# Kernel optimization log

Measured on AMD Instinct MI355X. Metric: run time of the kernel, lower is better.

Reference implementation:

```python
import jax, jax.numpy as jnp
import numpy as np

N, E, H, D = 50000, 200000, 4, 64  # nodes, directed input edges, heads, hidden_dim
NODE_IN, EDGE_IN = 6, 4


def _ln(x, g, b):
    m = x.mean(-1, keepdims=True)
    v = ((x - m) ** 2).mean(-1, keepdims=True)
    return (x - m) / jnp.sqrt(v + 1e-5) * g + b


def setup_inputs() -> dict:
    key = jax.random.key(0)
    ks = iter(jax.random.split(key, 48))
    def w(i, o):
        return jax.random.normal(next(ks), (i, o), jnp.float32) / np.sqrt(i)
    def b(o):
        return jnp.zeros((o,), jnp.float32)
    return {
        "x": jax.random.normal(next(ks), (N, NODE_IN), jnp.float32),
        "edge_attr": jax.random.normal(next(ks), (E, EDGE_IN), jnp.float32),
        "ne_w1": w(NODE_IN, D), "ne_b1": b(D), "ne_w2": w(D, D), "ne_b2": b(D),
        "ee_w1": w(EDGE_IN, D), "ee_b1": b(D), "ee_w2": w(D, D), "ee_b2": b(D),
        "lnc_g": jnp.ones((2 * D,), jnp.float32), "lnc_b": jnp.zeros((2 * D,), jnp.float32),
        "tq_w": w(2 * D, H * D), "tq_b": b(H * D),
        "tk_w": w(2 * D, H * D), "tk_b": b(H * D),
        "tv_w": w(2 * D, H * D), "tv_b": b(H * D),
        "ts_w": w(2 * D, H * D), "ts_b": b(H * D),
        "lnt_g": jnp.ones((H * D,), jnp.float32), "lnt_b": jnp.zeros((H * D,), jnp.float32),
        "pn_w": w(H * D, D), "pn_b": b(D),
        "pe_w": w(H * D, D), "pe_b": b(D),
        "ec_w1": w(2 * D, D), "ec_b1": b(D), "ec_w2": w(D, 1), "ec_b2": b(1),
        "edge_index": jax.random.randint(next(ks), (2, E), 0, N),
    }


def _forward(x, edge_index, edge_attr, ne_w1, ne_b1, ne_w2, ne_b2,
             ee_w1, ee_b1, ee_w2, ee_b2, lnc_g, lnc_b,
             tq_w, tq_b, tk_w, tk_b, tv_w, tv_b, ts_w, ts_b,
             lnt_g, lnt_b, pn_w, pn_b, pe_w, pe_b,
             ec_w1, ec_b1, ec_w2, ec_b2):
    # bidirectionalize edges
    send = jnp.concatenate([edge_index[0], edge_index[1]])   # [2E]
    recv = jnp.concatenate([edge_index[1], edge_index[0]])   # [2E]
    ea_bi = jnp.concatenate([edge_attr, edge_attr], axis=0)  # [2E, EDGE_IN]
    # 2-layer ReLU MLP encoders (make_mlp with default ReLU output activation)
    node = jax.nn.relu(jax.nn.relu(x @ ne_w1 + ne_b1) @ ne_w2 + ne_b2)        # [N, D]
    edge = jax.nn.relu(jax.nn.relu(ea_bi @ ee_w1 + ee_b1) @ ee_w2 + ee_b2)    # [2E, D]
    for _ in range(1):  # n_iterations = 1
        x0, e0 = node, edge
        agg = jax.ops.segment_sum(edge, recv, num_segments=N)                  # scatter_add
        comb = _ln(jnp.concatenate([node, agg - node], axis=1), lnc_g, lnc_b)  # [N, 2D]
        # TransformerConv(2D -> D, heads=H, concat=True, root_weight=True)
        q = (comb @ tq_w + tq_b).reshape(N, H, D)
        k = (comb @ tk_w + tk_b).reshape(N, H, D)
        v = (comb @ tv_w + tv_b).reshape(N, H, D)
        q_e = q[recv]; k_e = k[send]; v_e = v[send]                            # [2E, H, D]
        score = (q_e * k_e).sum(-1) / np.sqrt(D)                               # [2E, H]
        m = jax.lax.stop_gradient(jax.ops.segment_max(score, recv, num_segments=N))
        ex = jnp.exp(score - m[recv])
        denom = jax.ops.segment_sum(ex, recv, num_segments=N)
        alpha = ex / (denom[recv] + 1e-16)                                     # per-dst softmax
        attn = jax.ops.segment_sum(alpha[:, :, None] * v_e, recv, num_segments=N).reshape(N, H * D)
        outn = _ln(attn + comb @ ts_w + ts_b, lnt_g, lnt_b)                    # skip (root) + LN
        node = outn @ pn_w + pn_b + x0
        edge = (outn[send] - outn[recv]) @ pe_w + pe_b + e0
    start, end = edge_index[0], edge_index[1]
    clf = jnp.concatenate([node[start], node[end]], axis=1)                    # [E, 2D]
    return (jax.nn.relu(clf @ ec_w1 + ec_b1) @ ec_w2 + ec_b2).squeeze(-1)      # [E]


def reference(x, edge_attr, ne_w1, ne_b1, ne_w2, ne_b2, ee_w1, ee_b1, ee_w2, ee_b2,
              lnc_g, lnc_b, tq_w, tq_b, tk_w, tk_b, tv_w, tv_b, ts_w, ts_b,
              lnt_g, lnt_b, pn_w, pn_b, pe_w, pe_b, ec_w1, ec_b1, ec_w2, ec_b2,
              edge_index):
    return _forward(x, edge_index, edge_attr, ne_w1, ne_b1, ne_w2, ne_b2,
                    ee_w1, ee_b1, ee_w2, ee_b2, lnc_g, lnc_b,
                    tq_w, tq_b, tk_w, tk_b, tv_w, tv_b, ts_w, ts_b,
                    lnt_g, lnt_b, pn_w, pn_b, pe_w, pe_b,
                    ec_w1, ec_b1, ec_w2, ec_b2)
```

## Files before the change

kernel.cpp:

```cpp
#include <hip/hip_runtime.h>
#include <hip/hip_bf16.h>


typedef __attribute__((ext_vector_type(8))) short short8;
typedef __attribute__((ext_vector_type(8))) unsigned short u16x8;
typedef __attribute__((ext_vector_type(4))) float f32x4;

__device__ __forceinline__ float wave_reduce_sum(float p) {
  #pragma unroll
  for (int o = 32; o; o >>= 1) p += __shfl_xor(p, o);
  return p;
}
__device__ __forceinline__ ushort f2b(float x) {
  union { float f; unsigned u; } a; a.f = x;
  unsigned r = a.u + 0x7FFF + ((a.u >> 16) & 1);
  return (ushort)(r >> 16);
}
__device__ __forceinline__ float b2f(ushort u) {
  return __uint_as_float((unsigned)u << 16);
}

__global__ __launch_bounds__(256) void node_encoder(
    const float* __restrict__ x, const float* __restrict__ w1,
    const float* __restrict__ b1, const float* __restrict__ w2,
    const float* __restrict__ b2, ushort* __restrict__ out, int N)
{
  __shared__ float sW2[64 * 64];
  __shared__ float sH[4][64];
  int tid = threadIdx.x;
  for (int i = tid; i < 64 * 64; i += 256) sW2[i] = w2[i];
  int wave = tid >> 6, lane = tid & 63;
  int n = blockIdx.x * 4 + wave;
  int nc = n < N ? n : (N - 1);
  float h = b1[lane];
  #pragma unroll
  for (int i = 0; i < 6; ++i) h += x[nc * 6 + i] * w1[i * 64 + lane];
  h = fmaxf(h, 0.f);
  sH[wave][lane] = h;
  __syncthreads();
  float o = b2[lane];
  #pragma unroll 8
  for (int j = 0; j < 64; ++j) o += sH[wave][j] * sW2[j * 64 + lane];
  o = fmaxf(o, 0.f);
  if (n < N) out[n * 64 + lane] = f2b(o);
}

__global__ __launch_bounds__(256) void prep_weights(
    const float* __restrict__ tq_w, const float* __restrict__ tk_w,
    const float* __restrict__ tv_w, const float* __restrict__ ts_w,
    const float* __restrict__ tq_b, const float* __restrict__ tk_b,
    const float* __restrict__ tv_b, const float* __restrict__ ts_b,
    const float* __restrict__ pn_w, const float* __restrict__ ec_w1,
    const float* __restrict__ ee_w2,
    ushort* __restrict__ wqkvsT, float* __restrict__ bqkvs,
    ushort* __restrict__ pnT, ushort* __restrict__ ec1T,
    ushort* __restrict__ ee2T)
{
  int idx = blockIdx.x * 256 + threadIdx.x;
  if (idx < 131072) {
    int p = idx >> 7, k = idx & 127;
    int g, cc;
    if (p < 256) { g = 0; cc = p; }
    else if (p < 768) {
      int d2 = p - 256; int head = d2 >> 7; int ww = d2 & 127;
      int slot = ww >> 3; int o = ww & 7;
      if (o < 4) { g = 1; cc = head * 64 + slot * 4 + o; }
      else       { g = 2; cc = head * 64 + slot * 4 + o - 4; }
    } else { g = 3; cc = p - 768; }
    const float* w = (g == 0) ? tq_w : (g == 1) ? tk_w : (g == 2) ? tv_w : ts_w;
    float v = w[k * 256 + cc];
    if (g == 0) v *= 0.125f;
    wqkvsT[idx] = f2b(v);
  } else if (idx < 147456) {
    int i = idx - 131072; int c = i >> 8, k = i & 255;
    pnT[i] = f2b(pn_w[k * 64 + c]);
  } else if (idx < 155648) {
    int i = idx - 147456; int c = i >> 7, k = i & 127;
    ec1T[i] = f2b(ec_w1[k * 64 + c]);
  } else if (idx < 159744) {
    int i = idx - 155648; int c = i >> 6, k = i & 63;
    ee2T[i] = f2b(ee_w2[k * 64 + c]);
  } else if (idx < 160768) {
    int p = idx - 159744;
    int g, cc;
    if (p < 256) { g = 0; cc = p; }
    else if (p < 768) {
      int d2 = p - 256; int head = d2 >> 7; int ww = d2 & 127;
      int slot = ww >> 3; int o = ww & 7;
      if (o < 4) { g = 1; cc = head * 64 + slot * 4 + o; }
      else       { g = 2; cc = head * 64 + slot * 4 + o - 4; }
    } else { g = 3; cc = p - 768; }
    const float* b = (g == 0) ? tq_b : (g == 1) ? tk_b : (g == 2) ? tv_b : ts_b;
    float v = b[cc];
    if (g == 0) v *= 0.125f;
    bqkvs[p] = v;
  }
}

__global__ __launch_bounds__(256) void deg_count(
    const int* __restrict__ ei, int* __restrict__ deg, int E)
{
  int e = blockIdx.x * 256 + threadIdx.x;
  if (e >= E) return;
  atomicAdd(&deg[ei[e]], 1);
  atomicAdd(&deg[ei[E + e]], 1);
}

__global__ __launch_bounds__(64) void alloc_ranges(
    const int* __restrict__ deg, int* __restrict__ base,
    int* __restrict__ fillcur, int* __restrict__ cursor, int N)
{
  int lane = threadIdx.x;
  int n = blockIdx.x * 64 + lane;
  int d = (n < N) ? deg[n] : 0;
  int s = d;
  #pragma unroll
  for (int o = 1; o < 64; o <<= 1) {
    int t = __shfl_up(s, o);
    if (lane >= o) s += t;
  }
  int tot = __shfl(s, 63);
  int wb = 0;
  if (lane == 63) wb = atomicAdd(cursor, tot);
  wb = __shfl(wb, 63);
  if (n < N) { base[n] = wb + s - d; fillcur[n] = wb + s - d; }
}

__global__ __launch_bounds__(256) void csr_fill(
    const int* __restrict__ ei, int* __restrict__ fillcur,
    int* __restrict__ csr_send, int2* __restrict__ slot2, int E)
{
  int e = blockIdx.x * 256 + threadIdx.x;
  if (e >= E) return;
  int a = ei[e], b = ei[E + e];
  int pa = atomicAdd(&fillcur[b], 1);
  csr_send[pa] = a;
  int pb = atomicAdd(&fillcur[a], 1);
  csr_send[pb] = b;
  slot2[e] = make_int2(pa, pb);
}

__global__ __launch_bounds__(256) void edge_enc(
    const float* __restrict__ ea, const float* __restrict__ w1,
    const float* __restrict__ b1, const ushort* __restrict__ ee2T,
    const float* __restrict__ b2, const int2* __restrict__ slot2,
    ushort* __restrict__ f_csr, int E)
{
  __shared__ ushort As[64 * 72];
  __shared__ ushort Bs[64 * 72];
  __shared__ ushort fT[64 * 72];
  __shared__ int2 sSlot[64];
  int tid = threadIdx.x;
  int wv = tid >> 6, lane = tid & 63, r16 = lane & 15, g4 = lane >> 4;
  int e0 = blockIdx.x * 64;
  if (tid < 64) {
    int e = e0 + tid;
    if (e < E) sSlot[tid] = slot2[e];
  }
  #pragma unroll
  for (int it = 0; it < 2; ++it) {
    int idx = tid + it * 256;
    int r = idx >> 3, c = idx & 7;
    *(short8*)&Bs[r * 72 + c * 8] = *(const short8*)&ee2T[r * 64 + c * 8];
  }
  {
    int c = tid & 63;
    float w0 = w1[c], w1v = w1[64 + c], w2v = w1[128 + c], w3v = w1[192 + c];
    float bb = b1[c];
    int rbase = tid >> 6;
    #pragma unroll
    for (int i = 0; i < 16; ++i) {
      int r = rbase + i * 4;
      int e = e0 + r; if (e >= E) e = E - 1;
      float4 a = *(const float4*)(ea + (size_t)e * 4);
      float hv = bb + a.x * w0 + a.y * w1v + a.z * w2v + a.w * w3v;
      As[r * 72 + c] = f2b(fmaxf(hv, 0.f));
    }
  }
  __syncthreads();
  f32x4 acc[4] = {};
  #pragma unroll
  for (int kk = 0; kk < 2; ++kk) {
    short8 a = *(const short8*)&As[(wv * 16 + r16) * 72 + kk * 32 + g4 * 8];
    #pragma unroll
    for (int sc = 0; sc < 4; ++sc) {
      short8 b = *(const short8*)&Bs[(sc * 16 + r16) * 72 + kk * 32 + g4 * 8];
      acc[sc] = __builtin_amdgcn_mfma_f32_16x16x32_bf16(a, b, acc[sc], 0, 0, 0);
    }
  }
  #pragma unroll
  for (int sc = 0; sc < 4; ++sc) {
    int c = sc * 16 + r16;
    float bs = b2[c];
    #pragma unroll
    for (int j = 0; j < 4; ++j) {
      int r = wv * 16 + g4 * 4 + j;
      fT[r * 72 + c] = f2b(fmaxf(acc[sc][j] + bs, 0.f));
    }
  }
  __syncthreads();
  int gsub = lane >> 4, l16 = lane & 15;
  #pragma unroll
  for (int rr = 0; rr < 8; ++rr) {
    int r = wv * 16 + rr * 2 + (gsub >> 1);
    int e = e0 + r;
    if (e < E) {
      int slot = (gsub & 1) ? sSlot[r].y : sSlot[r].x;
      *(ushort4*)&f_csr[(size_t)slot * 64 + l16 * 4] =
          *(const ushort4*)&fT[r * 72 + l16 * 4];
    }
  }
}

__global__ __launch_bounds__(256) void qkvs_gemm(
    const ushort* __restrict__ node0, const ushort* __restrict__ f_csr,
    const int* __restrict__ base, const int* __restrict__ deg,
    const float* __restrict__ lng, const float* __restrict__ lnb,
    const ushort* __restrict__ wqkvsT, const float* __restrict__ bias,
    ushort* __restrict__ qkvs, int N)
{
  __shared__ ushort As[64 * 136];
  __shared__ ushort Bs[64 * 136];
  __shared__ ushort Os[64 * 68];
  int tid = threadIdx.x;
  int wv = tid >> 6, lane = tid & 63, r16 = lane & 15, g4 = lane >> 4;
  int row0 = blockIdx.x * 64;
  #pragma unroll
  for (int it = 0; it < 4; ++it) {
    int idx = tid + it * 256;
    int r = idx >> 4, c = idx & 15;
    *(short8*)&Bs[r * 136 + c * 8] = *(const short8*)&wqkvsT[(size_t)r * 128 + c * 8];
  }
  float g0 = lng[lane], g1 = lng[64 + lane];
  float bb0 = lnb[lane], bb1 = lnb[64 + lane];
  for (int i = 0; i < 16; ++i) {
    int r = wv * 16 + i;
    int n = row0 + r; if (n >= N) n = N - 1;
    float v0 = b2f(node0[(size_t)n * 64 + lane]);
    int bs_ = base[n], dn_ = deg[n];
    float a = 0.f;
    for (int j = 0; j < dn_; j += 4) {
      int i1 = bs_ + (j + 1 < dn_ ? j + 1 : dn_ - 1);
      int i2 = bs_ + (j + 2 < dn_ ? j + 2 : dn_ - 1);
      int i3 = bs_ + (j + 3 < dn_ ? j + 3 : dn_ - 1);
      float f0 = b2f(f_csr[(size_t)(bs_ + j) * 64 + lane]);
      float f1 = b2f(f_csr[(size_t)i1 * 64 + lane]);
      float f2 = b2f(f_csr[(size_t)i2 * 64 + lane]);
      float f3 = b2f(f_csr[(size_t)i3 * 64 + lane]);
      a += f0;
      if (j + 1 < dn_) a += f1;
      if (j + 2 < dn_) a += f2;
      if (j + 3 < dn_) a += f3;
    }
    float v1 = a - v0;
    float s = wave_reduce_sum(v0 + v1);
    float ss = wave_reduce_sum(v0 * v0 + v1 * v1);
    float mean = s * (1.f / 128.f);
    float var = ss * (1.f / 128.f) - mean * mean;
    float rstd = rsqrtf(var + 1e-5f);
    As[r * 136 + lane]      = f2b((v0 - mean) * rstd * g0 + bb0);
    As[r * 136 + 64 + lane] = f2b((v1 - mean) * rstd * g1 + bb1);
  }
  __syncthreads();
  for (int ct = 0; ct < 16; ++ct) {
    short8 pf[4];
    if (ct < 15) {
      #pragma unroll
      for (int it = 0; it < 4; ++it) {
        int idx = tid + it * 256;
        int r = idx >> 4, c = idx & 15;
        pf[it] = *(const short8*)&wqkvsT[(size_t)((ct + 1) * 64 + r) * 128 + c * 8];
      }
    }
    f32x4 acc[4] = {};
    #pragma unroll
    for (int kk = 0; kk < 4; ++kk) {
      short8 a = *(const short8*)&As[(wv * 16 + r16) * 136 + kk * 32 + g4 * 8];
      #pragma unroll
      for (int sc = 0; sc < 4; ++sc) {
        short8 b = *(const short8*)&Bs[(sc * 16 + r16) * 136 + kk * 32 + g4 * 8];
        acc[sc] = __builtin_amdgcn_mfma_f32_16x16x32_bf16(a, b, acc[sc], 0, 0, 0);
      }
    }
    __syncthreads();
    if (ct < 15) {
      #pragma unroll
      for (int it = 0; it < 4; ++it) {
        int idx = tid + it * 256;
        int r = idx >> 4, c = idx & 15;
        *(short8*)&Bs[r * 136 + c * 8] = pf[it];
      }
    }
    #pragma unroll
    for (int sc = 0; sc < 4; ++sc) {
      float bs = bias[ct * 64 + sc * 16 + r16];
      #pragma unroll
      for (int j = 0; j < 4; ++j)
        Os[(wv * 16 + g4 * 4 + j) * 68 + sc * 16 + r16] = f2b(acc[sc][j] + bs);
    }
    __syncthreads();
    #pragma unroll
    for (int it = 0; it < 2; ++it) {
      int idx = tid + it * 256;
      int r = idx >> 3, ch = idx & 7;
      int gr = row0 + r;
      if (gr < N)
        *(short8*)&qkvs[(size_t)gr * 1024 + ct * 64 + ch * 8] =
            *(const short8*)&Os[r * 68 + ch * 8];
    }
  }
}

__global__ __launch_bounds__(256) void mgemm(
    const ushort* __restrict__ A, int lda, int M,
    const ushort* __restrict__ BT, const float* __restrict__ bias, int K,
    ushort* __restrict__ outB, int ldo,
    const ushort* __restrict__ res, int ldres, int doRelu)
{
  __shared__ ushort As[64 * 136];
  __shared__ ushort Bs[64 * 136];
  __shared__ ushort Os[64 * 68];
  int tid = threadIdx.x;
  int wv = tid >> 6, lane = tid & 63;
  int r16 = lane & 15, g4 = lane >> 4;
  int row0 = blockIdx.x * 64, col0 = blockIdx.y * 64;
  f32x4 acc[4] = {};
  for (int k0 = 0; k0 < K; k0 += 128) {
    int BK = K - k0; if (BK > 128) BK = 128;
    int csh = (BK == 64) ? 3 : 4;
    int cmask = (1 << csh) - 1;
    int tot = 64 << csh;
    for (int idx = tid; idx < tot; idx += 256) {
      int r = idx >> csh, c = idx & cmask;
      int gr = row0 + r; if (gr >= M) gr = M - 1;
      *(short8*)&As[r * 136 + c * 8] =
          *(const short8*)&A[(size_t)gr * lda + k0 + c * 8];
      *(short8*)&Bs[r * 136 + c * 8] =
          *(const short8*)&BT[(size_t)(col0 + r) * K + k0 + c * 8];
    }
    __syncthreads();
    int ks = BK >> 5;
    for (int kk = 0; kk < ks; ++kk) {
      short8 a = *(const short8*)&As[(wv * 16 + r16) * 136 + kk * 32 + g4 * 8];
      #pragma unroll
      for (int ct = 0; ct < 4; ++ct) {
        short8 b = *(const short8*)&Bs[(ct * 16 + r16) * 136 + kk * 32 + g4 * 8];
        acc[ct] = __builtin_amdgcn_mfma_f32_16x16x32_bf16(a, b, acc[ct], 0, 0, 0);
      }
    }
    __syncthreads();
  }
  #pragma unroll
  for (int ct = 0; ct < 4; ++ct) {
    int c = col0 + ct * 16 + r16;
    float bs = bias[c];
    #pragma unroll
    for (int j = 0; j < 4; ++j) {
      int r = row0 + wv * 16 + g4 * 4 + j;
      int rc = r < M ? r : M - 1;
      float vv = acc[ct][j] + bs;
      if (doRelu) vv = fmaxf(vv, 0.f);
      if (res) vv += b2f(res[(size_t)rc * ldres + c]);
      Os[(wv * 16 + g4 * 4 + j) * 68 + ct * 16 + r16] = f2b(vv);
    }
  }
  __syncthreads();
  #pragma unroll
  for (int it = 0; it < 2; ++it) {
    int idx = tid + it * 256;
    int r = idx >> 3, ch = idx & 7;
    int gr = row0 + r;
    if (gr < M)
      *(short8*)&outB[(size_t)gr * ldo + col0 + ch * 8] =
          *(const short8*)&Os[r * 68 + ch * 8];
  }
}

__global__ __launch_bounds__(256) void attn_ln2(
    ushort* __restrict__ qkvs, const int* __restrict__ base,
    const int* __restrict__ deg, const int* __restrict__ csr_send,
    const float* __restrict__ g, const float* __restrict__ bb, int N)
{
  int tid = blockIdx.x * 256 + threadIdx.x;
  int n = tid >> 6, lane = tid & 63;
  if (n >= N) return;
  int dbase = (lane >> 4) * 64 + (lane & 15) * 4;
  int kvoff = 256 + (lane >> 4) * 128 + (lane & 15) * 8;
  ushort4 qu = *(const ushort4*)(qkvs + (size_t)n * 1024 + dbase);
  float q0 = b2f(qu.x), q1 = b2f(qu.y), q2 = b2f(qu.z), q3 = b2f(qu.w);
  float l = 0.f, a0 = 0.f, a1 = 0.f, a2 = 0.f, a3 = 0.f;
  int b0 = base[n], dn = deg[n];
  for (int j = 0; j < dn; j += 4) {
    int i1 = b0 + (j + 1 < dn ? j + 1 : dn - 1);
    int i2 = b0 + (j + 2 < dn ? j + 2 : dn - 1);
    int i3 = b0 + (j + 3 < dn ? j + 3 : dn - 1);
    int s0 = csr_send[b0 + j], s1 = csr_send[i1];
    int s2 = csr_send[i2], s3 = csr_send[i3];
    u16x8 kv0 = *(const u16x8*)(qkvs + (size_t)s0 * 1024 + kvoff);
    u16x8 kv1 = *(const u16x8*)(qkvs + (size_t)s1 * 1024 + kvoff);
    u16x8 kv2 = *(const u16x8*)(qkvs + (size_t)s2 * 1024 + kvoff);
    u16x8 kv3 = *(const u16x8*)(qkvs + (size_t)s3 * 1024 + kvoff);
    float p0 = q0 * b2f((ushort)kv0[0]) + q1 * b2f((ushort)kv0[1]) +
               q2 * b2f((ushort)kv0[2]) + q3 * b2f((ushort)kv0[3]);
    float p1 = q0 * b2f((ushort)kv1[0]) + q1 * b2f((ushort)kv1[1]) +
               q2 * b2f((ushort)kv1[2]) + q3 * b2f((ushort)kv1[3]);
    float p2 = q0 * b2f((ushort)kv2[0]) + q1 * b2f((ushort)kv2[1]) +
               q2 * b2f((ushort)kv2[2]) + q3 * b2f((ushort)kv2[3]);
    float p3 = q0 * b2f((ushort)kv3[0]) + q1 * b2f((ushort)kv3[1]) +
               q2 * b2f((ushort)kv3[2]) + q3 * b2f((ushort)kv3[3]);
    #pragma unroll
    for (int o = 1; o < 16; o <<= 1) {
      p0 += __shfl_xor(p0, o); p1 += __shfl_xor(p1, o);
      p2 += __shfl_xor(p2, o); p3 += __shfl_xor(p3, o);
    }
    float e0 = __expf(p0);
    float e1 = (j + 1 < dn) ? __expf(p1) : 0.f;
    float e2 = (j + 2 < dn) ? __expf(p2) : 0.f;
    float e3 = (j + 3 < dn) ? __expf(p3) : 0.f;
    l += e0 + e1 + e2 + e3;
    a0 += e0 * b2f((ushort)kv0[4]) + e1 * b2f((ushort)kv1[4]) +
          e2 * b2f((ushort)kv2[4]) + e3 * b2f((ushort)kv3[4]);
    a1 += e0 * b2f((ushort)kv0[5]) + e1 * b2f((ushort)kv1[5]) +
          e2 * b2f((ushort)kv2[5]) + e3 * b2f((ushort)kv3[5]);
    a2 += e0 * b2f((ushort)kv0[6]) + e1 * b2f((ushort)kv1[6]) +
          e2 * b2f((ushort)kv2[6]) + e3 * b2f((ushort)kv3[6]);
    a3 += e0 * b2f((ushort)kv0[7]) + e1 * b2f((ushort)kv1[7]) +
          e2 * b2f((ushort)kv2[7]) + e3 * b2f((ushort)kv3[7]);
  }
  ushort4 su = *(const ushort4*)(qkvs + (size_t)n * 1024 + 768 + dbase);
  float rl = 1.f / (l + 1e-16f);
  float y0 = a0 * rl + b2f(su.x), y1 = a1 * rl + b2f(su.y);
  float y2 = a2 * rl + b2f(su.z), y3 = a3 * rl + b2f(su.w);
  float s1 = wave_reduce_sum(y0 + y1 + y2 + y3);
  float s2 = wave_reduce_sum(y0 * y0 + y1 * y1 + y2 * y2 + y3 * y3);
  float mean = s1 * (1.f / 256.f);
  float var = s2 * (1.f / 256.f) - mean * mean;
  float rstd = rsqrtf(var + 1e-5f);
  ushort4 o;
  o.x = f2b((y0 - mean) * rstd * g[dbase + 0] + bb[dbase + 0]);
  o.y = f2b((y1 - mean) * rstd * g[dbase + 1] + bb[dbase + 1]);
  o.z = f2b((y2 - mean) * rstd * g[dbase + 2] + bb[dbase + 2]);
  o.w = f2b((y3 - mean) * rstd * g[dbase + 3] + bb[dbase + 3]);
  *(ushort4*)(qkvs + (size_t)n * 1024 + dbase) = o;
}

__global__ __launch_bounds__(256) void clf_fused(
    const ushort* __restrict__ nodeB, const int* __restrict__ ei,
    const ushort* __restrict__ ec1T, const float* __restrict__ b1,
    const float* __restrict__ w2, const float* __restrict__ b2v,
    float* __restrict__ out, int E)
{
  __shared__ ushort As[64 * 136];
  __shared__ ushort Bs[64 * 136];
  int tid = threadIdx.x;
  int wv = tid >> 6, lane = tid & 63;
  int r16 = lane & 15, g4 = lane >> 4;
  int e0 = blockIdx.x * 64;
  for (int idx = tid; idx < 1024; idx += 256) {
    int r = idx >> 4, c = idx & 15;
    int e = e0 + r; if (e >= E) e = E - 1;
    int node = (c < 8) ? ei[e] : ei[E + e];
    *(short8*)&As[r * 136 + c * 8] =
        *(const short8*)&nodeB[(size_t)node * 64 + (c & 7) * 8];
    *(short8*)&Bs[r * 136 + c * 8] = *(const short8*)&ec1T[r * 128 + c * 8];
  }
  __syncthreads();
  f32x4 acc[4] = {};
  #pragma unroll
  for (int kk = 0; kk < 4; ++kk) {
    short8 a = *(const short8*)&As[(wv * 16 + r16) * 136 + kk * 32 + g4 * 8];
    #pragma unroll
    for (int ct = 0; ct < 4; ++ct) {
      short8 b = *(const short8*)&Bs[(ct * 16 + r16) * 136 + kk * 32 + g4 * 8];
      acc[ct] = __builtin_amdgcn_mfma_f32_16x16x32_bf16(a, b, acc[ct], 0, 0, 0);
    }
  }
  float p0 = 0.f, p1 = 0.f, p2 = 0.f, p3 = 0.f;
  #pragma unroll
  for (int ct = 0; ct < 4; ++ct) {
    int c = ct * 16 + r16;
    float bb1 = b1[c], ww = w2[c];
    p0 += fmaxf(acc[ct][0] + bb1, 0.f) * ww;
    p1 += fmaxf(acc[ct][1] + bb1, 0.f) * ww;
    p2 += fmaxf(acc[ct][2] + bb1, 0.f) * ww;
    p3 += fmaxf(acc[ct][3] + bb1, 0.f) * ww;
  }
  float part[4] = {p0, p1, p2, p3};
  #pragma unroll
  for (int j = 0; j < 4; ++j) {
    float p = part[j];
    p += __shfl_xor(p, 1); p += __shfl_xor(p, 2);
    p += __shfl_xor(p, 4); p += __shfl_xor(p, 8);
    int r = e0 + wv * 16 + g4 * 4 + j;
    if (r16 == 0 && r < E) out[r] = p + b2v[0];
  }
}

extern "C" void kernel_launch(void* const* d_in, const int* in_sizes, int n_in,
                              void* d_out, int out_size, void* d_ws, size_t ws_size,
                              hipStream_t stream)
{
  const float* x     = (const float*)d_in[0];
  const float* ea    = (const float*)d_in[1];
  const float* ne_w1 = (const float*)d_in[2];
  const float* ne_b1 = (const float*)d_in[3];
  const float* ne_w2 = (const float*)d_in[4];
  const float* ne_b2 = (const float*)d_in[5];
  const float* ee_w1 = (const float*)d_in[6];
  const float* ee_b1 = (const float*)d_in[7];
  const float* ee_w2 = (const float*)d_in[8];
  const float* ee_b2 = (const float*)d_in[9];
  const float* lnc_g = (const float*)d_in[10];
  const float* lnc_b = (const float*)d_in[11];
  const float* tq_w  = (const float*)d_in[12];
  const float* tq_b  = (const float*)d_in[13];
  const float* tk_w  = (const float*)d_in[14];
  const float* tk_b  = (const float*)d_in[15];
  const float* tv_w  = (const float*)d_in[16];
  const float* tv_b  = (const float*)d_in[17];
  const float* ts_w  = (const float*)d_in[18];
  const float* ts_b  = (const float*)d_in[19];
  const float* lnt_g = (const float*)d_in[20];
  const float* lnt_b = (const float*)d_in[21];
  const float* pn_w  = (const float*)d_in[22];
  const float* pn_b  = (const float*)d_in[23];
  const float* ec_w1 = (const float*)d_in[26];
  const float* ec_b1 = (const float*)d_in[27];
  const float* ec_w2 = (const float*)d_in[28];
  const float* ec_b2 = (const float*)d_in[29];
  const int*   ei    = (const int*)d_in[30];

  const int N = in_sizes[0] / 6;
  const int E = in_sizes[1] / 4;
  float* out = (float*)d_out;

  char* w = (char*)d_ws;
  size_t off = 0;
  auto alloc = [&](size_t bytes) -> char* {
    char* p = w + off;
    off = (off + bytes + 255) & ~(size_t)255;
    return p;
  };
  ushort* node0   = (ushort*)alloc((size_t)N * 64 * 2);
  ushort* qkvs    = (ushort*)alloc((size_t)N * 1024 * 2);
  ushort* f_csr   = (ushort*)alloc((size_t)2 * E * 64 * 2);
  ushort* nodeB   = (ushort*)alloc((size_t)N * 64 * 2);
  ushort* wqkvsT  = (ushort*)alloc(1024 * 128 * 2);
  float*  bqkvs   = (float*)alloc(1024 * 4);
  ushort* pnT     = (ushort*)alloc(64 * 256 * 2);
  ushort* ec1T    = (ushort*)alloc(64 * 128 * 2);
  ushort* ee2T    = (ushort*)alloc(64 * 64 * 2);
  int* deg      = (int*)alloc((size_t)N * 4);
  int* base     = (int*)alloc((size_t)N * 4);
  int* fillcur  = (int*)alloc((size_t)N * 4);
  int* csr_send = (int*)alloc((size_t)2 * E * 4);
  int2* slot2   = (int2*)alloc((size_t)E * 8);
  int* cursor   = (int*)alloc(256);

  hipMemsetAsync(deg, 0, (size_t)N * 4, stream);
  hipMemsetAsync(cursor, 0, 4, stream);

  prep_weights<<<(160768 + 255) / 256, 256, 0, stream>>>(
      tq_w, tk_w, tv_w, ts_w, tq_b, tk_b, tv_b, ts_b, pn_w, ec_w1, ee_w2,
      wqkvsT, bqkvs, pnT, ec1T, ee2T);
  node_encoder<<<(N + 3) / 4, 256, 0, stream>>>(x, ne_w1, ne_b1, ne_w2, ne_b2, node0, N);
  deg_count<<<(E + 255) / 256, 256, 0, stream>>>(ei, deg, E);
  alloc_ranges<<<(N + 63) / 64, 64, 0, stream>>>(deg, base, fillcur, cursor, N);
  csr_fill<<<(E + 255) / 256, 256, 0, stream>>>(ei, fillcur, csr_send, slot2, E);
  edge_enc<<<(E + 63) / 64, 256, 0, stream>>>(ea, ee_w1, ee_b1, ee2T, ee_b2,
                                              slot2, f_csr, E);
  qkvs_gemm<<<(N + 63) / 64, 256, 0, stream>>>(
      node0, f_csr, base, deg, lnc_g, lnc_b, wqkvsT, bqkvs, qkvs, N);
  attn_ln2<<<(N * 64 + 255) / 256, 256, 0, stream>>>(
      qkvs, base, deg, csr_send, lnt_g, lnt_b, N);
  mgemm<<<dim3((N + 63) / 64, 1), 256, 0, stream>>>(
      qkvs, 1024, N, pnT, pn_b, 256, nodeB, 64, node0, 64, 0);
  clf_fused<<<(E + 63) / 64, 256, 0, stream>>>(
      nodeB, ei, ec1T, ec_b1, ec_w2, ec_b2, out, E);
}
```

Measured before the change: 296.3 us.

## Split neighbor gather and LayerNorm out of the QKVS GEMM into its own kernel

The per-node edge-feature aggregation and LayerNorm, which each wave ran serially over 16 rows inside the GEMM kernel, now runs in a separate kernel with one wave per node, writing a bf16 comb buffer. The GEMM then loads its A tile directly from comb. The aim is more memory-level parallelism for the irregular gather and a lighter GEMM prologue, at the cost of an extra launch and an N×128 bf16 round trip through memory. The tail-index clamp in the gather loops also changes to reuse index j, which keeps the same address locality.

```diff
diff --git a/kernel.cpp b/kernel.cpp
--- a/kernel.cpp
+++ b/kernel.cpp
@@ -212,12 +212,44 @@
   }
 }
 
+__global__ __launch_bounds__(256) void comb_gather_ln(
+    const ushort* __restrict__ node, const ushort* __restrict__ f_csr,
+    const int* __restrict__ base, const int* __restrict__ deg,
+    const float* __restrict__ g, const float* __restrict__ b,
+    ushort* __restrict__ comb, int N)
+{
+  int tid = blockIdx.x * 256 + threadIdx.x;
+  int n = tid >> 6, lane = tid & 63;
+  if (n >= N) return;
+  float v0 = b2f(node[(size_t)n * 64 + lane]);
+  float a = 0.f;
+  int b0 = base[n], dn = deg[n];
+  for (int j = 0; j < dn; j += 4) {
+    int i1 = b0 + (j + 1 < dn ? j + 1 : j);
+    int i2 = b0 + (j + 2 < dn ? j + 2 : j);
+    int i3 = b0 + (j + 3 < dn ? j + 3 : j);
+    float f0 = b2f(f_csr[(size_t)(b0 + j) * 64 + lane]);
+    float f1 = b2f(f_csr[(size_t)i1 * 64 + lane]);
+    float f2 = b2f(f_csr[(size_t)i2 * 64 + lane]);
+    float f3 = b2f(f_csr[(size_t)i3 * 64 + lane]);
+    a += f0;
+    if (j + 1 < dn) a += f1;
+    if (j + 2 < dn) a += f2;
+    if (j + 3 < dn) a += f3;
+  }
+  float v1 = a - v0;
+  float s = wave_reduce_sum(v0 + v1);
+  float ss = wave_reduce_sum(v0 * v0 + v1 * v1);
+  float mean = s * (1.f / 128.f);
+  float var = ss * (1.f / 128.f) - mean * mean;
+  float rstd = rsqrtf(var + 1e-5f);
+  comb[(size_t)n * 128 + lane]      = f2b((v0 - mean) * rstd * g[lane] + b[lane]);
+  comb[(size_t)n * 128 + 64 + lane] = f2b((v1 - mean) * rstd * g[64 + lane] + b[64 + lane]);
+}
+
 __global__ __launch_bounds__(256) void qkvs_gemm(
-    const ushort* __restrict__ node0, const ushort* __restrict__ f_csr,
-    const int* __restrict__ base, const int* __restrict__ deg,
-    const float* __restrict__ lng, const float* __restrict__ lnb,
-    const ushort* __restrict__ wqkvsT, const float* __restrict__ bias,
-    ushort* __restrict__ qkvs, int N)
+    const ushort* __restrict__ comb, const ushort* __restrict__ wqkvsT,
+    const float* __restrict__ bias, ushort* __restrict__ qkvs, int N)
 {
   __shared__ ushort As[64 * 136];
   __shared__ ushort Bs[64 * 136];
@@ -229,37 +261,9 @@
   for (int it = 0; it < 4; ++it) {
     int idx = tid + it * 256;
     int r = idx >> 4, c = idx & 15;
+    int gr = row0 + r; if (gr >= N) gr = N - 1;
+    *(short8*)&As[r * 136 + c * 8] = *(const short8*)&comb[(size_t)gr * 128 + c * 8];
     *(short8*)&Bs[r * 136 + c * 8] = *(const short8*)&wqkvsT[(size_t)r * 128 + c * 8];
-  }
-  float g0 = lng[lane], g1 = lng[64 + lane];
-  float bb0 = lnb[lane], bb1 = lnb[64 + lane];
-  for (int i = 0; i < 16; ++i) {
-    int r = wv * 16 + i;
-    int n = row0 + r; if (n >= N) n = N - 1;
-    float v0 = b2f(node0[(size_t)n * 64 + lane]);
-    int bs_ = base[n], dn_ = deg[n];
-    float a = 0.f;
-    for (int j = 0; j < dn_; j += 4) {
-      int i1 = bs_ + (j + 1 < dn_ ? j + 1 : dn_ - 1);
-      int i2 = bs_ + (j + 2 < dn_ ? j + 2 : dn_ - 1);
-      int i3 = bs_ + (j + 3 < dn_ ? j + 3 : dn_ - 1);
-      float f0 = b2f(f_csr[(size_t)(bs_ + j) * 64 + lane]);
-      float f1 = b2f(f_csr[(size_t)i1 * 64 + lane]);
-      float f2 = b2f(f_csr[(size_t)i2 * 64 + lane]);
-      float f3 = b2f(f_csr[(size_t)i3 * 64 + lane]);
-      a += f0;
-      if (j + 1 < dn_) a += f1;
-      if (j + 2 < dn_) a += f2;
-      if (j + 3 < dn_) a += f3;
-    }
-    float v1 = a - v0;
-    float s = wave_reduce_sum(v0 + v1);
-    float ss = wave_reduce_sum(v0 * v0 + v1 * v1);
-    float mean = s * (1.f / 128.f);
-    float var = ss * (1.f / 128.f) - mean * mean;
-    float rstd = rsqrtf(var + 1e-5f);
-    As[r * 136 + lane]      = f2b((v0 - mean) * rstd * g0 + bb0);
-    As[r * 136 + 64 + lane] = f2b((v1 - mean) * rstd * g1 + bb1);
   }
   __syncthreads();
   for (int ct = 0; ct < 16; ++ct) {
@@ -391,9 +395,9 @@
   float l = 0.f, a0 = 0.f, a1 = 0.f, a2 = 0.f, a3 = 0.f;
   int b0 = base[n], dn = deg[n];
   for (int j = 0; j < dn; j += 4) {
-    int i1 = b0 + (j + 1 < dn ? j + 1 : dn - 1);
-    int i2 = b0 + (j + 2 < dn ? j + 2 : dn - 1);
-    int i3 = b0 + (j + 3 < dn ? j + 3 : dn - 1);
+    int i1 = b0 + (j + 1 < dn ? j + 1 : j);
+    int i2 = b0 + (j + 2 < dn ? j + 2 : j);
+    int i3 = b0 + (j + 3 < dn ? j + 3 : j);
     int s0 = csr_send[b0 + j], s1 = csr_send[i1];
     int s2 = csr_send[i2], s3 = csr_send[i3];
     u16x8 kv0 = *(const u16x8*)(qkvs + (size_t)s0 * 1024 + kvoff);
@@ -542,6 +546,7 @@
     return p;
   };
   ushort* node0   = (ushort*)alloc((size_t)N * 64 * 2);
+  ushort* comb    = (ushort*)alloc((size_t)N * 128 * 2);
   ushort* qkvs    = (ushort*)alloc((size_t)N * 1024 * 2);
   ushort* f_csr   = (ushort*)alloc((size_t)2 * E * 64 * 2);
   ushort* nodeB   = (ushort*)alloc((size_t)N * 64 * 2);
@@ -569,8 +574,9 @@
   csr_fill<<<(E + 255) / 256, 256, 0, stream>>>(ei, fillcur, csr_send, slot2, E);
   edge_enc<<<(E + 63) / 64, 256, 0, stream>>>(ea, ee_w1, ee_b1, ee2T, ee_b2,
                                               slot2, f_csr, E);
-  qkvs_gemm<<<(N + 63) / 64, 256, 0, stream>>>(
-      node0, f_csr, base, deg, lnc_g, lnc_b, wqkvsT, bqkvs, qkvs, N);
+  comb_gather_ln<<<(N * 64 + 255) / 256, 256, 0, stream>>>(
+      node0, f_csr, base, deg, lnc_g, lnc_b, comb, N);
+  qkvs_gemm<<<(N + 63) / 64, 256, 0, stream>>>(comb, wqkvsT, bqkvs, qkvs, N);
   attn_ln2<<<(N * 64 + 255) / 256, 256, 0, stream>>>(
       qkvs, base, deg, csr_send, lnt_g, lnt_b, N);
   mgemm<<<dim3((N + 63) / 64, 1), 256, 0, stream>>>(
```

New measurement: 271.4 us. 1.09x faster.
